# Kernel tuning notes

Hardware: AMD Instinct MI355X
Metric: run time of the kernel (lower is better)

The kernel has to match this reference:

```python
import jax, jax.numpy as jnp
import numpy as np

BS, IN_CH, SEQ = 2, 512, 1024
DK, DV, H = 64, 64, 16


def setup_inputs() -> dict:
    key = jax.random.key(0)
    ks = jax.random.split(key, 8)
    # init scales mirror the torch init lambdas
    sq = IN_CH ** (-0.5) * DK ** (-0.25)            # initQ / initK
    sv = (1.0 / 0.012) * H ** (-0.5) * IN_CH ** (-0.5) * 40 ** (-0.5)  # initV
    sl = 0.5 * H ** (-0.5)                           # initL
    inp = jax.random.normal(ks[0], (BS, IN_CH, SEQ), jnp.float32)
    mask = jnp.zeros((BS, SEQ), jnp.float32)
    Wq = jax.random.normal(ks[1], (IN_CH, DK, H), jnp.float32) * sq
    Wk = jax.random.normal(ks[2], (IN_CH, DK, H), jnp.float32) * sq
    Wv = jax.random.normal(ks[3], (IN_CH, DV, H), jnp.float32) * sv
    Wl = jax.random.normal(ks[4], (H, H), jnp.float32) * sl
    Ww = jax.random.normal(ks[5], (H, H), jnp.float32) * 0.01
    Wo = jax.random.normal(ks[6], (DV * H, IN_CH), jnp.float32) * 0.03
    alpha = jnp.full((1,), 2.0, jnp.float32)
    return {"inp": inp, "mask": mask, "Wq": Wq, "Wk": Wk, "Wv": Wv,
            "alphaq": alpha, "alphak": alpha, "alphav": alpha,
            "Wl": Wl, "Ww": Ww, "Wo": Wo}


def reference(inp, mask, Wq, Wk, Wv, alphaq, alphak, alphav, Wl, Ww, Wo):
    # inp: (b, c_in, s); projections -> (b, d, s, h)
    Q = jax.nn.sigmoid(alphaq) * jnp.einsum('bcs,cdh->bdsh', inp, Wq)
    K = jax.nn.sigmoid(alphak) * jnp.einsum('bcs,cdh->bdsh', inp, Wk)
    V = jax.nn.sigmoid(alphav) * jnp.einsum('bcs,cdh->bdsh', inp, Wv)
    # per-head attention logits: (b, sq, sk, h)
    J = jnp.einsum('bdqh,bdkh->bqkh', Q, K)
    # pre-softmax head mixing, additive mask over key positions
    EL = jnp.einsum('bqkh,hg->bqkg', J, Wl) - mask[:, None, :, None]
    W = jax.nn.softmax(EL, axis=2)  # softmax over keys (dim 2)
    # post-softmax head mixing
    U = jnp.einsum('bqkg,gv->bqkv', W, Ww)
    # attend to values: (b, sq, dv, hv) -> (b, sq, dv*hv)
    O = jnp.einsum('bqkv,bdkv->bqdv', U, V)
    O = O.reshape(O.shape[0], O.shape[1], DV * H)
    # output projection, back to (b, out_dim, s)
    resid = jnp.einsum('bqc,cd->bdq', O, Wo)
    # shortcut is identity since out_dim == in_ch
    return inp + resid
```

## Files before the change

### kernel.cpp

```cpp
#include <hip/hip_runtime.h>
#include <hip/hip_bf16.h>


#define B_S  2
#define C_INN 512
#define SEQL 1024
#define D_K  64
#define N_H  16
#define BQJ  (2 * 1024 * 1024)
#define KSL  16
#define KSO  8

typedef __attribute__((ext_vector_type(4))) float floatx4;
typedef __attribute__((ext_vector_type(8))) short short8;
typedef __attribute__((ext_vector_type(2))) unsigned int uint2v;
typedef __fp16 h2raw __attribute__((ext_vector_type(2)));
typedef _Float16 f16x4 __attribute__((ext_vector_type(4)));

static __device__ __forceinline__ float bf2f(unsigned short u) {
  union { unsigned int i; float f; } x; x.i = ((unsigned int)u) << 16; return x.f;
}
static __device__ __forceinline__ unsigned short f2bf(float f) {
  union { float f; unsigned int i; } x; x.f = f;
  return (unsigned short)((x.i + 0x7fffu + ((x.i >> 16) & 1u)) >> 16);
}
static __device__ __forceinline__ unsigned int pkh2(float a, float b) {
  h2raw r = __builtin_amdgcn_cvt_pkrtz(a, b);
  union { h2raw h; unsigned int u; } x; x.h = r; return x.u;
}
static __device__ __forceinline__ unsigned int pkbf(float a, float b) {
  return (unsigned int)f2bf(a) | ((unsigned int)f2bf(b) << 16);
}
static __device__ __forceinline__ f16x4 mkh4(unsigned int a, unsigned int b) {
  union { unsigned int u[2]; f16x4 h; } x; x.u[0] = a; x.u[1] = b; return x.h;
}

__global__ __launch_bounds__(256) void ath_tr(
    const float* __restrict__ inp, const float* __restrict__ Wq,
    const float* __restrict__ Wk,  const float* __restrict__ Wv,
    const float* __restrict__ Wo,
    unsigned short* __restrict__ inpT, unsigned short* __restrict__ WT,
    unsigned short* __restrict__ WoT)
{
  const int z = blockIdx.z;
  const float* src; unsigned short* dst; int R, C;
  if      (z == 0) { src = inp;              dst = inpT;                R = 512;  C = 1024; }
  else if (z == 1) { src = inp + 512 * 1024; dst = inpT + 1024 * 512;   R = 512;  C = 1024; }
  else if (z == 2) { src = Wq;               dst = WT;                  R = 512;  C = 1024; }
  else if (z == 3) { src = Wk;               dst = WT + 1024 * 512;     R = 512;  C = 1024; }
  else if (z == 4) { src = Wv;               dst = WT + 2 * 1024 * 512; R = 512;  C = 1024; }
  else             { src = Wo;               dst = WoT;                 R = 1024; C = 512;  }
  const int ct = blockIdx.x, rt = blockIdx.y;
  if (ct * 32 >= C || rt * 32 >= R) return;

  __shared__ float Ts[32][33];
  const int t = threadIdx.x;
  {
    const int r = t >> 3, c4 = (t & 7) * 4;
    const floatx4 g = *(const floatx4*)(src + (size_t)(rt * 32 + r) * C + ct * 32 + c4);
    Ts[r][c4 + 0] = g[0]; Ts[r][c4 + 1] = g[1];
    Ts[r][c4 + 2] = g[2]; Ts[r][c4 + 3] = g[3];
  }
  __syncthreads();
  {
    const int i = t >> 3, k4 = (t & 7) * 4;
    const unsigned int o0 = pkbf(Ts[k4 + 0][i], Ts[k4 + 1][i]);
    const unsigned int o1 = pkbf(Ts[k4 + 2][i], Ts[k4 + 3][i]);
    *(uint2v*)(dst + (size_t)(ct * 32 + i) * R + rt * 32 + k4) = (uint2v){o0, o1};
  }
}

__global__ __launch_bounds__(256) void ath_qkv(
    const unsigned short* __restrict__ inpT,
    const unsigned short* __restrict__ WT,
    const float* __restrict__ Aq,
    const float* __restrict__ Ak,
    const float* __restrict__ Av,
    unsigned short* __restrict__ ws)
{
  const int sblk = blockIdx.x;
  const int nblk = blockIdx.y;
  const int z = blockIdx.z;
  const int b = z / 3, p = z % 3;
  const float* Ap = (p == 0) ? Aq : ((p == 1) ? Ak : Av);
  const float sig = 1.0f / (1.0f + __expf(-Ap[0]));

  __shared__ __align__(16) unsigned short As[64][40];
  __shared__ __align__(16) unsigned short Bs[64][40];

  const int tid = threadIdx.x;
  const int w = tid >> 6, lane = tid & 63;
  const int l15 = lane & 15, quad = lane >> 4;
  const int srow = tid >> 2, sc8 = (tid & 3) * 8;

  floatx4 acc[4];
#pragma unroll
  for (int i = 0; i < 4; ++i) acc[i] = (floatx4){0.f, 0.f, 0.f, 0.f};

  for (int cc = 0; cc < 16; ++cc) {
    const int c0 = cc * 32;
    __syncthreads();
    *(short8*)&As[srow][sc8] =
        *(const short8*)(inpT + ((size_t)(b * 1024 + sblk * 64 + srow)) * 512 + c0 + sc8);
    *(short8*)&Bs[srow][sc8] =
        *(const short8*)(WT + ((size_t)(p * 1024 + nblk * 64 + srow)) * 512 + c0 + sc8);
    __syncthreads();
    const short8 a = *(const short8*)&As[w * 16 + l15][quad * 8];
#pragma unroll
    for (int nt = 0; nt < 4; ++nt) {
      const short8 bb = *(const short8*)&Bs[nt * 16 + l15][quad * 8];
      acc[nt] = __builtin_amdgcn_mfma_f32_16x16x32_bf16(a, bb, acc[nt], 0, 0, 0);
    }
  }

  unsigned short* out = ws + (size_t)p * ((size_t)B_S * N_H * SEQL * D_K);
#pragma unroll
  for (int nt = 0; nt < 4; ++nt) {
    const int h = l15;
    const int d = nblk * 4 + nt;
#pragma unroll
    for (int r = 0; r < 4; ++r) {
      const int s = sblk * 64 + w * 16 + quad * 4 + r;
      const float vout = acc[nt][r] * sig;
      if (p == 2) out[((size_t)((b * N_H + h) * D_K + d)) * SEQL + s] = f2bf(vout);
      else        out[((size_t)((b * N_H + h) * SEQL + s)) * D_K + d] = f2bf(vout);
    }
  }
}

__global__ __launch_bounds__(256, 3) void ath_lpartP(
    const float* __restrict__ maskp,
    const float* __restrict__ Wl,
    const unsigned short* __restrict__ qkv,
    float* __restrict__ lp,
    unsigned short* __restrict__ Pws)
{
  const int qblk = blockIdx.x;
  const int ks   = blockIdx.y;
  const int b    = blockIdx.z;
  const int tid = threadIdx.x;
  const int w = tid >> 6, lane = tid & 63;
  const int l15 = lane & 15, quad = lane >> 4;

  const unsigned short* Qf = qkv;
  const unsigned short* Kf = qkv + (size_t)B_S * N_H * SEQL * D_K;

  __shared__ unsigned int JtU[9216];

  const f16x4 wlA = mkh4(pkh2(Wl[(quad * 4 + 0) * 16 + l15], Wl[(quad * 4 + 1) * 16 + l15]),
                         pkh2(Wl[(quad * 4 + 2) * 16 + l15], Wl[(quad * 4 + 3) * 16 + l15]));
  const f16x4 idB = mkh4(pkh2((quad * 4 + 0 == l15) ? 1.f : 0.f, (quad * 4 + 1 == l15) ? 1.f : 0.f),
                         pkh2((quad * 4 + 2 == l15) ? 1.f : 0.f, (quad * 4 + 3 == l15) ? 1.f : 0.f));
  const unsigned int ONE2 = 0x3C003C00u;
  const f16x4 onesB = mkh4(ONE2, ONE2);
  const f16x4 zeroB = mkh4(0u, 0u);

  const float mreg = maskp[b * SEQL + ks * 64 + w * 16 + l15];
  const int k0 = ks * 64;
  const int kabs = k0 + w * 16 + l15;

  short8 qf0[4], qf1[4];
#pragma unroll
  for (int hh = 0; hh < 4; ++hh) {
    const unsigned short* qb =
        Qf + ((size_t)((b * N_H + w * 4 + hh) * SEQL) + qblk * 16 + l15) * D_K;
    qf0[hh] = *(const short8*)(qb + quad * 8);
    qf1[hh] = *(const short8*)(qb + 32 + quad * 8);
  }

#pragma unroll
  for (int kt = 0; kt < 4; ++kt) {
    floatx4 jc[4];
#pragma unroll
    for (int hh = 0; hh < 4; ++hh) {
      const unsigned short* kb =
          Kf + ((size_t)((b * N_H + w * 4 + hh) * SEQL) + k0 + kt * 16 + l15) * D_K;
      const short8 kf0 = *(const short8*)(kb + quad * 8);
      const short8 kf1 = *(const short8*)(kb + 32 + quad * 8);
      floatx4 c = (floatx4){0.f, 0.f, 0.f, 0.f};
      c = __builtin_amdgcn_mfma_f32_16x16x32_bf16(qf0[hh], kf0, c, 0, 0, 0);
      c = __builtin_amdgcn_mfma_f32_16x16x32_bf16(qf1[hh], kf1, c, 0, 0, 0);
      jc[hh] = c;
    }
#pragma unroll
    for (int r = 0; r < 4; ++r) {
      const int base = ((quad * 4 + r) * 64 + kt * 16 + l15) * 9 + w * 2;
      JtU[base + 0] = pkh2(jc[0][r], jc[1][r]);
      JtU[base + 1] = pkh2(jc[2][r], jc[3][r]);
    }
  }

  __syncthreads();

  unsigned int* Pu = (unsigned int*)Pws;
  floatx4 dl0 = (floatx4){0.f, 0.f, 0.f, 0.f};
  floatx4 dl1 = (floatx4){0.f, 0.f, 0.f, 0.f};
#pragma unroll 4
  for (int q = 0; q < 16; ++q) {
    const int jb = (q * 64 + w * 16 + l15) * 9 + quad * 2;
    const f16x4 bj = mkh4(JtU[jb], JtU[jb + 1]);
    floatx4 d1 = __builtin_amdgcn_mfma_f32_16x16x16f16(
        wlA, bj, (floatx4){0.f, 0.f, 0.f, 0.f}, 0, 0, 0);
    float p[4];
#pragma unroll
    for (int r = 0; r < 4; ++r) {
      const float e = fminf(fmaxf(d1[r] - mreg, -60.f), 60.f);
      p[r] = __expf(e);
    }
    const unsigned int u0 = pkh2(p[0], p[1]);
    const unsigned int u1 = pkh2(p[2], p[3]);
    const size_t pidx =
        ((size_t)(b * 1024 + qblk * 16 + q) * 1024 + kabs) * 8 + quad * 2;
    *(uint2v*)&Pu[pidx] = (uint2v){u0, u1};

    const f16x4 ap = mkh4(u0, u1);
    floatx4 dt = __builtin_amdgcn_mfma_f32_16x16x16f16(
        ap, idB, (floatx4){0.f, 0.f, 0.f, 0.f}, 0, 0, 0);
    const f16x4 a2 = mkh4(pkh2(dt[0], dt[1]), pkh2(dt[2], dt[3]));
    const f16x4 eq = (l15 == q) ? onesB : zeroB;
    if (q & 1) dl1 = __builtin_amdgcn_mfma_f32_16x16x16f16(a2, eq, dl1, 0, 0, 0);
    else       dl0 = __builtin_amdgcn_mfma_f32_16x16x16f16(a2, eq, dl0, 0, 0, 0);
  }
  const floatx4 dl = dl0 + dl1;

  *(floatx4*)(lp + ((size_t)((ks * 4 + w) * 2 + b)) * 16384 +
              (size_t)(qblk * 16 + l15) * 16 + quad * 4) = dl;
}

__global__ __launch_bounds__(256, 3) void ath_lpart(
    const float* __restrict__ maskp,
    const float* __restrict__ Wl,
    const unsigned short* __restrict__ qkv,
    float* __restrict__ lp)
{
  const int qblk = blockIdx.x;
  const int ks   = blockIdx.y;
  const int b    = blockIdx.z;
  const int tid = threadIdx.x;
  const int w = tid >> 6, lane = tid & 63;
  const int l15 = lane & 15, quad = lane >> 4;

  const unsigned short* Qf = qkv;
  const unsigned short* Kf = qkv + (size_t)B_S * N_H * SEQL * D_K;

  __shared__ unsigned int JtU[9216];

  const f16x4 wlA = mkh4(pkh2(Wl[(quad * 4 + 0) * 16 + l15], Wl[(quad * 4 + 1) * 16 + l15]),
                         pkh2(Wl[(quad * 4 + 2) * 16 + l15], Wl[(quad * 4 + 3) * 16 + l15]));
  const f16x4 idB = mkh4(pkh2((quad * 4 + 0 == l15) ? 1.f : 0.f, (quad * 4 + 1 == l15) ? 1.f : 0.f),
                         pkh2((quad * 4 + 2 == l15) ? 1.f : 0.f, (quad * 4 + 3 == l15) ? 1.f : 0.f));
  const unsigned int ONE2 = 0x3C003C00u;
  const f16x4 onesB = mkh4(ONE2, ONE2);
  const f16x4 zeroB = mkh4(0u, 0u);

  const float mreg = maskp[b * SEQL + ks * 64 + w * 16 + l15];
  const int k0 = ks * 64;

  short8 qf0[4], qf1[4];
#pragma unroll
  for (int hh = 0; hh < 4; ++hh) {
    const unsigned short* qb =
        Qf + ((size_t)((b * N_H + w * 4 + hh) * SEQL) + qblk * 16 + l15) * D_K;
    qf0[hh] = *(const short8*)(qb + quad * 8);
    qf1[hh] = *(const short8*)(qb + 32 + quad * 8);
  }

#pragma unroll
  for (int kt = 0; kt < 4; ++kt) {
    floatx4 jc[4];
#pragma unroll
    for (int hh = 0; hh < 4; ++hh) {
      const unsigned short* kb =
          Kf + ((size_t)((b * N_H + w * 4 + hh) * SEQL) + k0 + kt * 16 + l15) * D_K;
      const short8 kf0 = *(const short8*)(kb + quad * 8);
      const short8 kf1 = *(const short8*)(kb + 32 + quad * 8);
      floatx4 c = (floatx4){0.f, 0.f, 0.f, 0.f};
      c = __builtin_amdgcn_mfma_f32_16x16x32_bf16(qf0[hh], kf0, c, 0, 0, 0);
      c = __builtin_amdgcn_mfma_f32_16x16x32_bf16(qf1[hh], kf1, c, 0, 0, 0);
      jc[hh] = c;
    }
#pragma unroll
    for (int r = 0; r < 4; ++r) {
      const int base = ((quad * 4 + r) * 64 + kt * 16 + l15) * 9 + w * 2;
      JtU[base + 0] = pkh2(jc[0][r], jc[1][r]);
      JtU[base + 1] = pkh2(jc[2][r], jc[3][r]);
    }
  }

  __syncthreads();

  floatx4 dl0 = (floatx4){0.f, 0.f, 0.f, 0.f};
  floatx4 dl1 = (floatx4){0.f, 0.f, 0.f, 0.f};
#pragma unroll 4
  for (int q = 0; q < 16; ++q) {
    const int jb = (q * 64 + w * 16 + l15) * 9 + quad * 2;
    const f16x4 bj = mkh4(JtU[jb], JtU[jb + 1]);
    floatx4 d1 = __builtin_amdgcn_mfma_f32_16x16x16f16(
        wlA, bj, (floatx4){0.f, 0.f, 0.f, 0.f}, 0, 0, 0);
    float p[4];
#pragma unroll
    for (int r = 0; r < 4; ++r) {
      const float e = fminf(fmaxf(d1[r] - mreg, -60.f), 60.f);
      p[r] = __expf(e);
    }
    const f16x4 ap = mkh4(pkh2(p[0], p[1]), pkh2(p[2], p[3]));
    floatx4 dt = __builtin_amdgcn_mfma_f32_16x16x16f16(
        ap, idB, (floatx4){0.f, 0.f, 0.f, 0.f}, 0, 0, 0);
    const f16x4 a2 = mkh4(pkh2(dt[0], dt[1]), pkh2(dt[2], dt[3]));
    const f16x4 eq = (l15 == q) ? onesB : zeroB;
    if (q & 1) dl1 = __builtin_amdgcn_mfma_f32_16x16x16f16(a2, eq, dl1, 0, 0, 0);
    else       dl0 = __builtin_amdgcn_mfma_f32_16x16x16f16(a2, eq, dl0, 0, 0, 0);
  }
  const floatx4 dl = dl0 + dl1;

  *(floatx4*)(lp + ((size_t)((ks * 4 + w) * 2 + b)) * 16384 +
              (size_t)(qblk * 16 + l15) * 16 + quad * 4) = dl;
}

__global__ __launch_bounds__(256) void ath_linv(
    const float* __restrict__ lp, float* __restrict__ invl)
{
  const int t = blockIdx.x * 256 + threadIdx.x;
  const int b = t >> 14, rem = t & 16383;
  float s = 0.f;
#pragma unroll
  for (int sl = 0; sl < KSL * 4; ++sl) s += lp[(size_t)(sl * 2 + b) * 16384 + rem];
  invl[t] = 1.0f / fmaxf(s, 1e-37f);
}

__global__ __launch_bounds__(256, 2) void ath_opartP(
    const unsigned short* __restrict__ Pws,
    const float* __restrict__ Ww,
    const unsigned short* __restrict__ qkv,
    const float* __restrict__ invl,
    unsigned short* __restrict__ Obp)
{
  const int qblk = blockIdx.x;
  const int ks   = blockIdx.y;
  const int b    = blockIdx.z;
  const int tid = threadIdx.x;
  const int w = tid >> 6, lane = tid & 63;
  const int l15 = lane & 15, quad = lane >> 4;

  const unsigned short* Vf = qkv + 2 * (size_t)B_S * N_H * SEQL * D_K;

  __shared__ __align__(16) unsigned short Us[16 * 16 * 64];
  __shared__ float invls[16][16];

  invls[tid >> 4][tid & 15] =
      invl[(size_t)b * 16384 + (qblk * 16 + (tid >> 4)) * 16 + (tid & 15)];

  const f16x4 wwB = mkh4(pkh2(Ww[(quad * 4 + 0) * 16 + l15], Ww[(quad * 4 + 1) * 16 + l15]),
                         pkh2(Ww[(quad * 4 + 2) * 16 + l15], Ww[(quad * 4 + 3) * 16 + l15]));

  floatx4 oacc[4][4];
#pragma unroll
  for (int a = 0; a < 4; ++a)
#pragma unroll
    for (int d = 0; d < 4; ++d) oacc[a][d] = (floatx4){0.f, 0.f, 0.f, 0.f};

  const unsigned int* Pu = (const unsigned int*)Pws;

  __syncthreads();

  for (int rd = 0; rd < 2; ++rd) {
    const int kabs = ks * 128 + rd * 64 + w * 16 + l15;

#pragma unroll
    for (int qh = 0; qh < 2; ++qh) {
      uint2v pv[8];
#pragma unroll
      for (int qq = 0; qq < 8; ++qq) {
        const size_t pidx =
            ((size_t)(b * 1024 + qblk * 16 + qh * 8 + qq) * 1024 + kabs) * 8 + quad * 2;
        pv[qq] = *(const uint2v*)&Pu[pidx];
      }
#pragma unroll
      for (int qq = 0; qq < 8; ++qq) {
        const int q = qh * 8 + qq;
        const floatx4 iq = *(const floatx4*)&invls[q][quad * 4];
        union { unsigned int u; _Float16 h[2]; } z0, z1;
        z0.u = pv[qq][0]; z1.u = pv[qq][1];
        const f16x4 ap = mkh4(pkh2((float)z0.h[0] * iq[0], (float)z0.h[1] * iq[1]),
                              pkh2((float)z1.h[0] * iq[2], (float)z1.h[1] * iq[3]));
        floatx4 d2 = __builtin_amdgcn_mfma_f32_16x16x16f16(
            ap, wwB, (floatx4){0.f, 0.f, 0.f, 0.f}, 0, 0, 0);
        const int row = l15 * 16 + q;
        const int ch = (w * 2 + (quad >> 1)) ^ ((l15 ^ q) & 7);
        *(uint2v*)&Us[row * 64 + ch * 8 + (quad & 1) * 4] =
            (uint2v){pkbf(d2[0], d2[1]), pkbf(d2[2], d2[3])};
      }
    }

    __syncthreads();

#pragma unroll
    for (int tp = 0; tp < 2; ++tp) {
      const int kt_abs = ks * 128 + rd * 64 + tp * 32;
#pragma unroll
      for (int vv = 0; vv < 4; ++vv) {
        const int v = w * 4 + vv;
        const int ch = (tp * 4 + quad) ^ ((v ^ l15) & 7);
        const short8 ufr = *(const short8*)&Us[(v * 16 + l15) * 64 + ch * 8];
#pragma unroll
        for (int dt = 0; dt < 4; ++dt) {
          const short8 vfr = *(const short8*)(Vf +
              ((size_t)((b * N_H + v) * D_K + dt * 16 + l15)) * SEQL + kt_abs + quad * 8);
          oacc[vv][dt] = __builtin_amdgcn_mfma_f32_16x16x32_bf16(ufr, vfr, oacc[vv][dt], 0, 0, 0);
        }
      }
    }

    __syncthreads();
  }

#pragma unroll
  for (int vv = 0; vv < 4; ++vv) {
    const int v = w * 4 + vv;
#pragma unroll
    for (int dt = 0; dt < 4; ++dt) {
      const int d = dt * 16 + l15;
#pragma unroll
      for (int r = 0; r < 4; ++r) {
        const int q = qblk * 16 + quad * 4 + r;
        Obp[(size_t)ks * BQJ + ((size_t)(b * SEQL + q)) * 1024 + d * 16 + v] = f2bf(oacc[vv][dt][r]);
      }
    }
  }
}

__global__ __launch_bounds__(256, 2) void ath_opart(
    const float* __restrict__ maskp,
    const float* __restrict__ Wl,
    const float* __restrict__ Ww,
    const unsigned short* __restrict__ qkv,
    const float* __restrict__ invl,
    unsigned short* __restrict__ Obp)
{
  const int qblk = blockIdx.x;
  const int ks   = blockIdx.y;
  const int b    = blockIdx.z;
  const int tid = threadIdx.x;
  const int w = tid >> 6, lane = tid & 63;
  const int l15 = lane & 15, quad = lane >> 4;

  const unsigned short* Qf = qkv;
  const unsigned short* Kf = qkv + (size_t)B_S * N_H * SEQL * D_K;
  const unsigned short* Vf = qkv + 2 * (size_t)B_S * N_H * SEQL * D_K;

  __shared__ unsigned int JtU[9216];
  __shared__ float invls[16][16];

  invls[tid >> 4][tid & 15] =
      invl[(size_t)b * 16384 + (qblk * 16 + (tid >> 4)) * 16 + (tid & 15)];

  const f16x4 wlA = mkh4(pkh2(Wl[(quad * 4 + 0) * 16 + l15], Wl[(quad * 4 + 1) * 16 + l15]),
                         pkh2(Wl[(quad * 4 + 2) * 16 + l15], Wl[(quad * 4 + 3) * 16 + l15]));
  const f16x4 wwB = mkh4(pkh2(Ww[(quad * 4 + 0) * 16 + l15], Ww[(quad * 4 + 1) * 16 + l15]),
                         pkh2(Ww[(quad * 4 + 2) * 16 + l15], Ww[(quad * 4 + 3) * 16 + l15]));

  short8 qf0[4], qf1[4];
#pragma unroll
  for (int hh = 0; hh < 4; ++hh) {
    const unsigned short* qb =
        Qf + ((size_t)((b * N_H + w * 4 + hh) * SEQL) + qblk * 16 + l15) * D_K;
    qf0[hh] = *(const short8*)(qb + quad * 8);
    qf1[hh] = *(const short8*)(qb + 32 + quad * 8);
  }

  floatx4 oacc[4][4];
#pragma unroll
  for (int a = 0; a < 4; ++a)
#pragma unroll
    for (int d = 0; d < 4; ++d) oacc[a][d] = (floatx4){0.f, 0.f, 0.f, 0.f};

  __syncthreads();

  for (int rd = 0; rd < 2; ++rd) {
    const int k0 = ks * 128 + rd * 64;
    const float mreg = maskp[b * SEQL + k0 + w * 16 + l15];

#pragma unroll
    for (int kt = 0; kt < 4; ++kt) {
      floatx4 jc[4];
#pragma unroll
      for (int hh = 0; hh < 4; ++hh) {
        const unsigned short* kb =
            Kf + ((size_t)((b * N_H + w * 4 + hh) * SEQL) + k0 + kt * 16 + l15) * D_K;
        const short8 kf0 = *(const short8*)(kb + quad * 8);
        const short8 kf1 = *(const short8*)(kb + 32 + quad * 8);
        floatx4 c = (floatx4){0.f, 0.f, 0.f, 0.f};
        c = __builtin_amdgcn_mfma_f32_16x16x32_bf16(qf0[hh], kf0, c, 0, 0, 0);
        c = __builtin_amdgcn_mfma_f32_16x16x32_bf16(qf1[hh], kf1, c, 0, 0, 0);
        jc[hh] = c;
      }
#pragma unroll
      for (int r = 0; r < 4; ++r) {
        const int base = ((quad * 4 + r) * 64 + kt * 16 + l15) * 9 + w * 2;
        JtU[base + 0] = pkh2(jc[0][r], jc[1][r]);
        JtU[base + 1] = pkh2(jc[2][r], jc[3][r]);
      }
    }

    __syncthreads();

#pragma unroll 4
    for (int q = 0; q < 16; ++q) {
      const int jb = (q * 64 + w * 16 + l15) * 9 + quad * 2;
      const f16x4 bj = mkh4(JtU[jb], JtU[jb + 1]);
      floatx4 d1 = __builtin_amdgcn_mfma_f32_16x16x16f16(
          wlA, bj, (floatx4){0.f, 0.f, 0.f, 0.f}, 0, 0, 0);
      const floatx4 iq = *(const floatx4*)&invls[q][quad * 4];
      float p[4];
#pragma unroll
      for (int r = 0; r < 4; ++r) {
        const float e = fminf(fmaxf(d1[r] - mreg, -60.f), 60.f);
        p[r] = __expf(e) * iq[r];
      }
      const f16x4 ap = mkh4(pkh2(p[0], p[1]), pkh2(p[2], p[3]));
      floatx4 d2 = __builtin_amdgcn_mfma_f32_16x16x16f16(
          ap, wwB, (floatx4){0.f, 0.f, 0.f, 0.f}, 0, 0, 0);
      const int ub = (q * 64 + w * 16) * 9 + ((l15 + q) & 15) * 8 + quad * 2;
      *(uint2v*)&JtU[ub] = (uint2v){pkbf(d2[0], d2[1]), pkbf(d2[2], d2[3])};
    }

    __syncthreads();

    const unsigned short* JtS = (const unsigned short*)JtU;
#pragma unroll
    for (int tp = 0; tp < 2; ++tp) {
      const int kt_abs = ks * 128 + rd * 64 + tp * 32;
#pragma unroll
      for (int vv = 0; vv < 4; ++vv) {
        const int v = w * 4 + vv;
        const int wp = tp * 2 + (quad >> 1);
        const int so = (l15 * 64 + wp * 16) * 18 + ((v + l15) & 15) * 16 + (quad & 1) * 8;
        const short8 ufr = *(const short8*)&JtS[so];
#pragma unroll
        for (int dt = 0; dt < 4; ++dt) {
          const short8 vfr = *(const short8*)(Vf +
              ((size_t)((b * N_H + v) * D_K + dt * 16 + l15)) * SEQL + kt_abs + quad * 8);
          oacc[vv][dt] = __builtin_amdgcn_mfma_f32_16x16x32_bf16(ufr, vfr, oacc[vv][dt], 0, 0, 0);
        }
      }
    }

    __syncthreads();
  }

#pragma unroll
  for (int vv = 0; vv < 4; ++vv) {
    const int v = w * 4 + vv;
#pragma unroll
    for (int dt = 0; dt < 4; ++dt) {
      const int d = dt * 16 + l15;
#pragma unroll
      for (int r = 0; r < 4; ++r) {
        const int q = qblk * 16 + quad * 4 + r;
        Obp[(size_t)ks * BQJ + ((size_t)(b * SEQL + q)) * 1024 + d * 16 + v] = f2bf(oacc[vv][dt][r]);
      }
    }
  }
}

__global__ __launch_bounds__(256) void ath_osum(
    const unsigned short* __restrict__ Obp,
    unsigned short* __restrict__ Obsum)
{
  const size_t i = ((size_t)blockIdx.x * 256 + threadIdx.x) * 8;
  float a[8];
#pragma unroll
  for (int e = 0; e < 8; ++e) a[e] = 0.f;
#pragma unroll
  for (int ks = 0; ks < KSO; ++ks) {
    const short8 v = *(const short8*)(Obp + (size_t)ks * BQJ + i);
#pragma unroll
    for (int e = 0; e < 8; ++e) a[e] += bf2f((unsigned short)v[e]);
  }
  short8 o;
#pragma unroll
  for (int e = 0; e < 8; ++e) o[e] = (short)f2bf(a[e]);
  *(short8*)(Obsum + i) = o;
}

__global__ __launch_bounds__(256) void ath_out(
    const float* __restrict__ inp,
    const unsigned short* __restrict__ WoT,
    const unsigned short* __restrict__ Ob,
    float* __restrict__ out)
{
  const int qblk = blockIdx.x;
  const int cblk = blockIdx.y;
  const int b    = blockIdx.z;
  const int tid = threadIdx.x;
  const int w = tid >> 6, lane = tid & 63;
  const int l15 = lane & 15, quad = lane >> 4;

  __shared__ __align__(16) unsigned short Os[64][40];
  __shared__ __align__(16) unsigned short Wt[64][40];

  floatx4 acc[4];
#pragma unroll
  for (int i = 0; i < 4; ++i) acc[i] = (floatx4){0.f, 0.f, 0.f, 0.f};

  const int srow = tid >> 2, sj8 = (tid & 3) * 8;

  for (int jc = 0; jc < 32; ++jc) {
    const int j0 = jc * 32;
    __syncthreads();
    *(short8*)&Os[srow][sj8] =
        *(const short8*)(Ob + ((size_t)(b * SEQL + qblk * 64 + srow)) * 1024 + j0 + sj8);
    *(short8*)&Wt[srow][sj8] =
        *(const short8*)(WoT + ((size_t)(cblk * 64 + srow)) * 1024 + j0 + sj8);
    __syncthreads();
    const short8 a = *(const short8*)&Os[w * 16 + l15][quad * 8];
#pragma unroll
    for (int nt = 0; nt < 4; ++nt) {
      const short8 bb = *(const short8*)&Wt[nt * 16 + l15][quad * 8];
      acc[nt] = __builtin_amdgcn_mfma_f32_16x16x32_bf16(a, bb, acc[nt], 0, 0, 0);
    }
  }

#pragma unroll
  for (int nt = 0; nt < 4; ++nt) {
    const int co = cblk * 64 + nt * 16 + l15;
    const int qb = qblk * 64 + w * 16 + quad * 4;
    const float* ip = inp + ((size_t)(b * 512 + co)) * SEQL + qb;
    float* op = out + ((size_t)(b * 512 + co)) * SEQL + qb;
#pragma unroll
    for (int r = 0; r < 4; ++r) op[r] = acc[nt][r] + ip[r];
  }
}

extern "C" void kernel_launch(void* const* d_in, const int* in_sizes, int n_in,
                              void* d_out, int out_size, void* d_ws, size_t ws_size,
                              hipStream_t stream) {
  (void)in_sizes; (void)n_in; (void)out_size;
  const float* inp   = (const float*)d_in[0];
  const float* maskp = (const float*)d_in[1];
  const float* Wq    = (const float*)d_in[2];
  const float* Wk    = (const float*)d_in[3];
  const float* Wv    = (const float*)d_in[4];
  const float* Aq    = (const float*)d_in[5];
  const float* Ak    = (const float*)d_in[6];
  const float* Av    = (const float*)d_in[7];
  const float* Wl    = (const float*)d_in[8];
  const float* Ww    = (const float*)d_in[9];
  const float* Wo    = (const float*)d_in[10];

  const size_t MB = 1u << 20;
  unsigned short* qkv   = (unsigned short*)d_ws;
  unsigned short* Obsum = (unsigned short*)((char*)d_ws + 12 * MB);
  float*          invl  = (float*)((char*)d_ws + 16 * MB);
  unsigned short* WoT   = (unsigned short*)((char*)d_ws + 17 * MB);
  float*          lp    = (float*)((char*)d_ws + 18 * MB);
  unsigned short* WT    = (unsigned short*)((char*)d_ws + 26 * MB);
  unsigned short* inpT  = (unsigned short*)((char*)d_ws + 29 * MB);
  unsigned short* Obp   = (unsigned short*)((char*)d_ws + 18 * MB);
  unsigned short* Pws   = (unsigned short*)((char*)d_ws + 50 * MB);
  float* out = (float*)d_out;

  const bool useP = ws_size >= (size_t)114 * MB;

  ath_tr<<<dim3(32, 32, 6), 256, 0, stream>>>(inp, Wq, Wk, Wv, Wo, inpT, WT, WoT);
  ath_qkv<<<dim3(16, 16, 6), 256, 0, stream>>>(inpT, WT, Aq, Ak, Av, qkv);
  if (useP) {
    ath_lpartP<<<dim3(64, KSL, 2), 256, 0, stream>>>(maskp, Wl, qkv, lp, Pws);
    ath_linv<<<dim3(128), 256, 0, stream>>>(lp, invl);
    ath_opartP<<<dim3(64, KSO, 2), 256, 0, stream>>>(Pws, Ww, qkv, invl, Obp);
  } else {
    ath_lpart<<<dim3(64, KSL, 2), 256, 0, stream>>>(maskp, Wl, qkv, lp);
    ath_linv<<<dim3(128), 256, 0, stream>>>(lp, invl);
    ath_opart<<<dim3(64, KSO, 2), 256, 0, stream>>>(maskp, Wl, Ww, qkv, invl, Obp);
  }
  ath_osum<<<dim3(1024), 256, 0, stream>>>(Obp, Obsum);
  ath_out<<<dim3(16, 8, 2), 256, 0, stream>>>(inp, WoT, Obsum, out);
}
```

Measured before the change: 255.4 us.

## Split opart into single-wave blocks per head group without barriers

Replaces the 4-wave output-partial kernel with single-wave blocks indexed by batch and value-head group, so each wave computes the 16-head post-softmax mixing itself and keeps it in a small padded LDS buffer without block barriers. The V product switches to f16 MFMA, converting bf16 V in registers. This removes synchronisation and raises block count, but repeats P loads and mixing MFMAs four times across head groups and adds conversion work and some precision change.

```diff
diff --git a/kernel.cpp b/kernel.cpp
--- a/kernel.cpp
+++ b/kernel.cpp
@@ -328,7 +328,7 @@
   invl[t] = 1.0f / fmaxf(s, 1e-37f);
 }
 
-__global__ __launch_bounds__(256, 2) void ath_opartP(
+__global__ __launch_bounds__(64, 3) void ath_opart1w(
     const unsigned short* __restrict__ Pws,
     const float* __restrict__ Ww,
     const unsigned short* __restrict__ qkv,
@@ -337,18 +337,20 @@
 {
   const int qblk = blockIdx.x;
   const int ks   = blockIdx.y;
-  const int b    = blockIdx.z;
-  const int tid = threadIdx.x;
-  const int w = tid >> 6, lane = tid & 63;
+  const int z    = blockIdx.z;
+  const int b = z >> 2, vg = z & 3;
+  const int lane = threadIdx.x;
   const int l15 = lane & 15, quad = lane >> 4;
 
   const unsigned short* Vf = qkv + 2 * (size_t)B_S * N_H * SEQL * D_K;
 
-  __shared__ __align__(16) unsigned short Us[16 * 16 * 64];
+  __shared__ unsigned int Ul[2240];
   __shared__ float invls[16][16];
 
-  invls[tid >> 4][tid & 15] =
-      invl[(size_t)b * 16384 + (qblk * 16 + (tid >> 4)) * 16 + (tid & 15)];
+  {
+    const floatx4 g = *(const floatx4*)(invl + (size_t)b * 16384 + qblk * 256 + lane * 4);
+    *(floatx4*)&invls[(lane * 4) >> 4][(lane * 4) & 15] = g;
+  }
 
   const f16x4 wwB = mkh4(pkh2(Ww[(quad * 4 + 0) * 16 + l15], Ww[(quad * 4 + 1) * 16 + l15]),
                          pkh2(Ww[(quad * 4 + 2) * 16 + l15], Ww[(quad * 4 + 3) * 16 + l15]));
@@ -360,63 +362,45 @@
     for (int d = 0; d < 4; ++d) oacc[a][d] = (floatx4){0.f, 0.f, 0.f, 0.f};
 
   const unsigned int* Pu = (const unsigned int*)Pws;
-
-  __syncthreads();
-
-  for (int rd = 0; rd < 2; ++rd) {
-    const int kabs = ks * 128 + rd * 64 + w * 16 + l15;
-
-#pragma unroll
-    for (int qh = 0; qh < 2; ++qh) {
-      uint2v pv[8];
-#pragma unroll
-      for (int qq = 0; qq < 8; ++qq) {
-        const size_t pidx =
-            ((size_t)(b * 1024 + qblk * 16 + qh * 8 + qq) * 1024 + kabs) * 8 + quad * 2;
-        pv[qq] = *(const uint2v*)&Pu[pidx];
+  const size_t prow = (size_t)(b * 1024 + qblk * 16);
+
+  for (int kc8 = 0; kc8 < 8; ++kc8) {
+    const int kc = ks * 128 + kc8 * 16;
+
+#pragma unroll
+    for (int q = 0; q < 16; ++q) {
+      const uint2v pv = *(const uint2v*)&Pu[((prow + q) * 1024 + kc + l15) * 8 + quad * 2];
+      const floatx4 iq = *(const floatx4*)&invls[q][quad * 4];
+      union { unsigned int u; _Float16 h[2]; } z0, z1;
+      z0.u = pv[0]; z1.u = pv[1];
+      const f16x4 ap = mkh4(pkh2((float)z0.h[0] * iq[0], (float)z0.h[1] * iq[1]),
+                            pkh2((float)z1.h[0] * iq[2], (float)z1.h[1] * iq[3]));
+      floatx4 d2 = __builtin_amdgcn_mfma_f32_16x16x16f16(
+          ap, wwB, (floatx4){0.f, 0.f, 0.f, 0.f}, 0, 0, 0);
+      Ul[(quad * 2 + 0) * 280 + q * 17 + l15] = pkh2(d2[0], d2[1]);
+      Ul[(quad * 2 + 1) * 280 + q * 17 + l15] = pkh2(d2[2], d2[3]);
+    }
+
+#pragma unroll
+    for (int vv = 0; vv < 4; ++vv) {
+      const int v = vg * 4 + vv;
+      const f16x4 aU = mkh4(Ul[(quad * 2 + 0) * 280 + l15 * 17 + v],
+                            Ul[(quad * 2 + 1) * 280 + l15 * 17 + v]);
+#pragma unroll
+      for (int dt = 0; dt < 4; ++dt) {
+        const uint2v vu = *(const uint2v*)(Vf +
+            ((size_t)((b * N_H + v) * D_K + dt * 16 + l15)) * SEQL + kc + quad * 4);
+        union { uint2v u; unsigned short s[4]; } vz; vz.u = vu;
+        const f16x4 bV = mkh4(pkh2(bf2f(vz.s[0]), bf2f(vz.s[1])),
+                              pkh2(bf2f(vz.s[2]), bf2f(vz.s[3])));
+        oacc[vv][dt] = __builtin_amdgcn_mfma_f32_16x16x16f16(aU, bV, oacc[vv][dt], 0, 0, 0);
       }
-#pragma unroll
-      for (int qq = 0; qq < 8; ++qq) {
-        const int q = qh * 8 + qq;
-        const floatx4 iq = *(const floatx4*)&invls[q][quad * 4];
-        union { unsigned int u; _Float16 h[2]; } z0, z1;
-        z0.u = pv[qq][0]; z1.u = pv[qq][1];
-        const f16x4 ap = mkh4(pkh2((float)z0.h[0] * iq[0], (float)z0.h[1] * iq[1]),
-                              pkh2((float)z1.h[0] * iq[2], (float)z1.h[1] * iq[3]));
-        floatx4 d2 = __builtin_amdgcn_mfma_f32_16x16x16f16(
-            ap, wwB, (floatx4){0.f, 0.f, 0.f, 0.f}, 0, 0, 0);
-        const int row = l15 * 16 + q;
-        const int ch = (w * 2 + (quad >> 1)) ^ ((l15 ^ q) & 7);
-        *(uint2v*)&Us[row * 64 + ch * 8 + (quad & 1) * 4] =
-            (uint2v){pkbf(d2[0], d2[1]), pkbf(d2[2], d2[3])};
-      }
-    }
-
-    __syncthreads();
-
-#pragma unroll
-    for (int tp = 0; tp < 2; ++tp) {
-      const int kt_abs = ks * 128 + rd * 64 + tp * 32;
-#pragma unroll
-      for (int vv = 0; vv < 4; ++vv) {
-        const int v = w * 4 + vv;
-        const int ch = (tp * 4 + quad) ^ ((v ^ l15) & 7);
-        const short8 ufr = *(const short8*)&Us[(v * 16 + l15) * 64 + ch * 8];
-#pragma unroll
-        for (int dt = 0; dt < 4; ++dt) {
-          const short8 vfr = *(const short8*)(Vf +
-              ((size_t)((b * N_H + v) * D_K + dt * 16 + l15)) * SEQL + kt_abs + quad * 8);
-          oacc[vv][dt] = __builtin_amdgcn_mfma_f32_16x16x32_bf16(ufr, vfr, oacc[vv][dt], 0, 0, 0);
-        }
-      }
-    }
-
-    __syncthreads();
+    }
   }
 
 #pragma unroll
   for (int vv = 0; vv < 4; ++vv) {
-    const int v = w * 4 + vv;
+    const int v = vg * 4 + vv;
 #pragma unroll
     for (int dt = 0; dt < 4; ++dt) {
       const int d = dt * 16 + l15;
@@ -667,7 +651,7 @@
   if (useP) {
     ath_lpartP<<<dim3(64, KSL, 2), 256, 0, stream>>>(maskp, Wl, qkv, lp, Pws);
     ath_linv<<<dim3(128), 256, 0, stream>>>(lp, invl);
-    ath_opartP<<<dim3(64, KSO, 2), 256, 0, stream>>>(Pws, Ww, qkv, invl, Obp);
+    ath_opart1w<<<dim3(64, KSO, 8), 64, 0, stream>>>(Pws, Ww, qkv, invl, Obp);
   } else {
     ath_lpart<<<dim3(64, KSL, 2), 256, 0, stream>>>(maskp, Wl, qkv, lp);
     ath_linv<<<dim3(128), 256, 0, stream>>>(lp, invl);
```

Result: slower. 363.1 us (+42.2%).
